# Performance work log

Hardware: AMD Instinct MI355X
Metric: run time of the kernel (lower is better)

The kernel has to match this reference:

```python
import jax, jax.numpy as jnp
import numpy as np

H = 64
N_PERSON = 200000
N_MOVIE = 100000
E_ACTED = 1600000
E_DIRECTED = 200000
E_WWW = 3200000
N_LAYERS = 2


def setup_inputs() -> dict:
    key = jax.random.key(0)
    ks = jax.random.split(key, 24)
    s = 1.0 / np.sqrt(H)
    inp = {
        "x_person": jax.random.normal(ks[0], (N_PERSON, H), jnp.float32),
        "x_movie": jax.random.normal(ks[1], (N_MOVIE, H), jnp.float32),
        "acted_src": jax.random.randint(ks[2], (E_ACTED,), 0, N_PERSON, jnp.int32),
        "acted_dst": jax.random.randint(ks[3], (E_ACTED,), 0, N_MOVIE, jnp.int32),
        "directed_src": jax.random.randint(ks[4], (E_DIRECTED,), 0, N_PERSON, jnp.int32),
        "directed_dst": jax.random.randint(ks[5], (E_DIRECTED,), 0, N_MOVIE, jnp.int32),
        "www_src": jax.random.randint(ks[6], (E_WWW,), 0, N_PERSON, jnp.int32),
        "www_dst": jax.random.randint(ks[7], (E_WWW,), 0, N_PERSON, jnp.int32),
        # per-relation SAGEConv params, stacked over the 2 layers
        "Wl_acted": jax.random.normal(ks[8], (N_LAYERS, H, H), jnp.float32) * s,
        "bl_acted": jnp.zeros((N_LAYERS, H), jnp.float32),
        "Wr_acted": jax.random.normal(ks[9], (N_LAYERS, H, H), jnp.float32) * s,
        "Wl_directed": jax.random.normal(ks[10], (N_LAYERS, H, H), jnp.float32) * s,
        "bl_directed": jnp.zeros((N_LAYERS, H), jnp.float32),
        "Wr_directed": jax.random.normal(ks[11], (N_LAYERS, H, H), jnp.float32) * s,
        "Wl_www": jax.random.normal(ks[12], (N_LAYERS, H, H), jnp.float32) * s,
        "bl_www": jnp.zeros((N_LAYERS, H), jnp.float32),
        "Wr_www": jax.random.normal(ks[13], (N_LAYERS, H, H), jnp.float32) * s,
        "lin_W": jax.random.normal(ks[14], (1, H), jnp.float32) * s,
        "lin_b": jnp.zeros((1,), jnp.float32),
    }
    return inp


def sage_conv(x_src, x_dst, src, dst, Wl, bl, Wr, n_dst):
    # PyG SAGEConv: mean-aggregate source feats at dst, then lin_l(agg) + lin_r(x_dst)
    agg = jax.ops.segment_sum(x_src[src], dst, num_segments=n_dst)  # [n_dst, H_in]
    cnt = jax.ops.segment_sum(jnp.ones((src.shape[0],), x_src.dtype), dst, num_segments=n_dst)
    mean = agg / jnp.maximum(cnt, 1.0)[:, None]
    return mean @ Wl.T + bl + x_dst @ Wr.T


def reference(x_person, x_movie, acted_src, acted_dst, directed_src, directed_dst,
              www_src, www_dst, Wl_acted, bl_acted, Wr_acted,
              Wl_directed, bl_directed, Wr_directed,
              Wl_www, bl_www, Wr_www, lin_W, lin_b):
    x_p, x_m = x_person, x_movie
    for l in range(N_LAYERS):
        # HeteroConv(aggr='sum'): movie receives sum of acted_in and directed convs
        out_m = sage_conv(x_p, x_m, acted_src, acted_dst,
                          Wl_acted[l], bl_acted[l], Wr_acted[l], N_MOVIE)
        out_m = out_m + sage_conv(x_p, x_m, directed_src, directed_dst,
                                  Wl_directed[l], bl_directed[l], Wr_directed[l], N_MOVIE)
        out_p = sage_conv(x_p, x_p, www_src, www_dst,
                          Wl_www[l], bl_www[l], Wr_www[l], N_PERSON)
        x_m = jax.nn.relu(out_m)
        x_p = jax.nn.relu(out_p)
    return (x_m @ lin_W.T + lin_b).squeeze(-1)  # [N_MOVIE]
```

## Files before the change

kernel.cpp:

```cpp
#include <hip/hip_runtime.h>

#define H 64
#define N_PERSON 200000
#define N_MOVIE 100000
#define E_ACTED 1600000
#define E_DIRECTED 200000
#define E_WWW 3200000
#define E_TOTAL (E_ACTED + E_DIRECTED + E_WWW)

#define SH 11
#define NBIN 2048
#define CH 16384

static __device__ __forceinline__ ushort f2bf(float f) {
  uint u = __float_as_uint(f);
  uint r = (u + 0x7FFFu + ((u >> 16) & 1u)) >> 16;
  return (ushort)r;
}
static __device__ __forceinline__ float bflo(uint u) { return __uint_as_float(u << 16); }
static __device__ __forceinline__ float bfhi(uint u) { return __uint_as_float(u & 0xFFFF0000u); }
static __device__ __forceinline__ float bfhiq(uint u) { return __uint_as_float(u); }
static __device__ __forceinline__ uint packbf(float lo, float hi) {
  return (uint)f2bf(lo) | ((uint)f2bf(hi) << 16);
}


struct RelP {
  const int* src; const int* dst; int* off;
  int E, N, nblk, nbuk, blkbase, bukbase, cbase, ebase;
};


static __global__ __launch_bounds__(256) void cast_all_k(const float* __restrict__ i0,
                                                         ushort* __restrict__ o0, int n0,
                                                         const float* __restrict__ i1,
                                                         ushort* __restrict__ o1, int n1) {
  int i = blockIdx.x * 256 + threadIdx.x;
  int stride = gridDim.x * 256;
  int nt = n0 + n1;
  for (; i < nt; i += stride) {
    const float4* in; ushort4* out; int idx;
    if (i < n0) { in = (const float4*)i0; out = (ushort4*)o0; idx = i; }
    else { in = (const float4*)i1; out = (ushort4*)o1; idx = i - n0; }
    float4 v = in[idx];
    ushort4 o;
    o.x = f2bf(v.x); o.y = f2bf(v.y); o.z = f2bf(v.z); o.w = f2bf(v.w);
    out[idx] = o;
  }
}


static __global__ __launch_bounds__(1024) void scan_block_k(const int* __restrict__ in, int n,
                                                            int* __restrict__ out,
                                                            int* __restrict__ partials) {
  __shared__ int sm[1024];
  int tid = threadIdx.x;
  int gid = blockIdx.x * 1024 + tid;
  int v = (gid < n) ? in[gid] : 0;
  sm[tid] = v;
  __syncthreads();
  for (int d = 1; d < 1024; d <<= 1) {
    int t = (tid >= d) ? sm[tid - d] : 0;
    __syncthreads();
    if (tid >= d) sm[tid] += t;
    __syncthreads();
  }
  if (gid < n) out[gid] = sm[tid] - v;
  if (tid == 1023 && partials) partials[blockIdx.x] = sm[1023];
}

static __global__ __launch_bounds__(1024) void add_off_k(int* __restrict__ off, int n,
                                                         const int* __restrict__ parts, int total) {
  int gid = blockIdx.x * 1024 + threadIdx.x;
  if (gid < n) off[gid] += parts[gid >> 10];
  else if (gid == n) off[gid] = total;
}


static __global__ __launch_bounds__(256) void part_count_all_k(RelP a, RelP b, RelP c,
                                                               int* __restrict__ counts) {
  __shared__ int hist[128];
  int blk = blockIdx.x, t = threadIdx.x;
  RelP r = (blk >= c.blkbase) ? c : (blk >= b.blkbase) ? b : a;
  int lb = blk - r.blkbase;
  for (int i = t; i < r.nbuk; i += 256) hist[i] = 0;
  __syncthreads();
  int e0 = lb * CH, e1 = min(e0 + CH, r.E);
  for (int e = e0 + t; e < e1; e += 256) atomicAdd(&hist[r.dst[e] >> SH], 1);
  __syncthreads();
  for (int i = t; i < r.nbuk; i += 256) counts[r.cbase + i * r.nblk + lb] = hist[i];
}

static __global__ __launch_bounds__(256) void part_scatter_all_k(RelP a, RelP b, RelP c,
                                                                 const int* __restrict__ off_bb,
                                                                 int* __restrict__ pairs) {
  __shared__ int cur[128];
  int blk = blockIdx.x, t = threadIdx.x;
  RelP r = (blk >= c.blkbase) ? c : (blk >= b.blkbase) ? b : a;
  int lb = blk - r.blkbase;
  for (int i = t; i < r.nbuk; i += 256) cur[i] = off_bb[r.cbase + i * r.nblk + lb];
  __syncthreads();
  int e0 = lb * CH, e1 = min(e0 + CH, r.E);
  int e = e0 + t;
  for (; e + 256 < e1; e += 512) {
    int d0 = r.dst[e], s0 = r.src[e];
    int d1 = r.dst[e + 256], s1 = r.src[e + 256];
    int p0 = atomicAdd(&cur[d0 >> SH], 1);
    int p1 = atomicAdd(&cur[d1 >> SH], 1);
    pairs[p0] = ((d0 & (NBIN - 1)) << 18) | s0;
    pairs[p1] = ((d1 & (NBIN - 1)) << 18) | s1;
  }
  if (e < e1) {
    int d0 = r.dst[e], s0 = r.src[e];
    int p0 = atomicAdd(&cur[d0 >> SH], 1);
    pairs[p0] = ((d0 & (NBIN - 1)) << 18) | s0;
  }
}

static __global__ __launch_bounds__(1024) void fine_sort_all_k(RelP a, RelP b, RelP c,
                                                               const int* __restrict__ off_bb,
                                                               const int* __restrict__ pairs,
                                                               int* __restrict__ csr) {
  __shared__ int hist[NBIN];
  __shared__ int sc[NBIN];
  int bb = blockIdx.x, t = threadIdx.x;
  RelP r = (bb >= c.bukbase) ? c : (bb >= b.bukbase) ? b : a;
  int bkt = bb - r.bukbase;
  int bstart = off_bb[r.cbase + bkt * r.nblk];
  int bend = (bkt + 1 < r.nbuk) ? off_bb[r.cbase + (bkt + 1) * r.nblk] : (r.ebase + r.E);
  int base = bkt << SH;
  hist[t] = 0; hist[t + 1024] = 0;
  __syncthreads();
  for (int e = bstart + t; e < bend; e += 1024) atomicAdd(&hist[((uint)pairs[e]) >> 18], 1);
  __syncthreads();
  sc[t] = hist[t]; sc[t + 1024] = hist[t + 1024];
  __syncthreads();
  for (int d = 1; d < NBIN; d <<= 1) {
    int v0 = (t >= d) ? sc[t - d] : 0;
    int v1 = (t + 1024 >= d) ? sc[t + 1024 - d] : 0;
    __syncthreads();
    sc[t] += v0; sc[t + 1024] += v1;
    __syncthreads();
  }
  int ex0 = sc[t] - hist[t];
  int ex1 = sc[t + 1024] - hist[t + 1024];
  if (base + t < r.N) r.off[base + t] = bstart + ex0;
  if (base + t + 1024 < r.N) r.off[base + t + 1024] = bstart + ex1;
  if (bkt == r.nbuk - 1 && t == 0) r.off[r.N] = r.ebase + r.E;
  hist[t] = ex0; hist[t + 1024] = ex1;
  __syncthreads();
  for (int e = bstart + t; e < bend; e += 1024) {
    int p = pairs[e];
    int pos = bstart + atomicAdd(&hist[((uint)p) >> 18], 1);
    csr[pos] = p & 0x3FFFF;
  }
}


struct PullT { const ushort* xsrc; const int* off; ushort* mean; int n; int blkbase; };

static __global__ __launch_bounds__(256) void pull_all_k(PullT t0, PullT t1, PullT t2,
                                                         const int* __restrict__ csr) {
  int blk = blockIdx.x;
  PullT tk;
  if (t2.n > 0 && blk >= t2.blkbase) tk = t2;
  else if (blk >= t1.blkbase) tk = t1;
  else tk = t0;
  int lane = threadIdx.x & 63;
  int g = lane >> 3;
  int fo = lane & 7;
  int d = ((blk - tk.blkbase) * 4 + (threadIdx.x >> 6)) * 8 + g;
  bool dok = d < tk.n;
  int dd = dok ? d : (tk.n - 1);
  int e0 = tk.off[dd];
  int e1 = tk.off[dd + 1];
  int cnt = dok ? (e1 - e0) : 0;
  int mx = cnt;
  mx = max(mx, __shfl_xor(mx, 8, 64));
  mx = max(mx, __shfl_xor(mx, 16, 64));
  mx = max(mx, __shfl_xor(mx, 32, 64));

  const ushort* __restrict__ xrow = tk.xsrc + fo * 8;
  float a0 = 0.f, a1 = 0.f, a2 = 0.f, a3 = 0.f, a4 = 0.f, a5 = 0.f, a6 = 0.f, a7 = 0.f;

  int i = 0;
  for (; i + 2 <= mx; i += 2) {
    if (i + 1 < cnt) {
      int s0 = csr[e0 + i];
      int s1 = csr[e0 + i + 1];
      uint4 u0 = *(const uint4*)(xrow + (size_t)s0 * 64);
      uint4 u1 = *(const uint4*)(xrow + (size_t)s1 * 64);
      a0 += bflo(u0.x); a1 += bfhiq(u0.x);
      a2 += bflo(u0.y); a3 += bfhiq(u0.y);
      a4 += bflo(u0.z); a5 += bfhiq(u0.z);
      a6 += bflo(u0.w); a7 += bfhiq(u0.w);
      a0 += bflo(u1.x); a1 += bfhiq(u1.x);
      a2 += bflo(u1.y); a3 += bfhiq(u1.y);
      a4 += bflo(u1.z); a5 += bfhiq(u1.z);
      a6 += bflo(u1.w); a7 += bfhiq(u1.w);
    } else if (i < cnt) {
      int s0 = csr[e0 + i];
      uint4 u0 = *(const uint4*)(xrow + (size_t)s0 * 64);
      a0 += bflo(u0.x); a1 += bfhiq(u0.x);
      a2 += bflo(u0.y); a3 += bfhiq(u0.y);
      a4 += bflo(u0.z); a5 += bfhiq(u0.z);
      a6 += bflo(u0.w); a7 += bfhiq(u0.w);
    }
  }
  if (i < mx && i < cnt) {
    int s0 = csr[e0 + i];
    uint4 u0 = *(const uint4*)(xrow + (size_t)s0 * 64);
    a0 += bflo(u0.x); a1 += bfhiq(u0.x);
    a2 += bflo(u0.y); a3 += bfhiq(u0.y);
    a4 += bflo(u0.z); a5 += bfhiq(u0.z);
    a6 += bflo(u0.w); a7 += bfhiq(u0.w);
  }

  if (dok) {
    float inv = 1.0f / fmaxf((float)cnt, 1.0f);
    uint4 o;
    o.x = packbf(a0 * inv, a1 * inv);
    o.y = packbf(a2 * inv, a3 * inv);
    o.z = packbf(a4 * inv, a5 * inv);
    o.w = packbf(a6 * inv, a7 * inv);
    *(uint4*)(tk.mean + (size_t)d * 64 + fo * 8) = o;
  }
}


struct GemmT {
  const ushort *A0, *A1, *A2;
  const float *W0, *W1, *W2, *Wadd, *b0, *b1;
  ushort* outB;
  const float *projW, *projb;
  float* projOut;
  int M, nsrc, blkbase;
};

static __global__ __launch_bounds__(256) void gemm_all_k(GemmT g0, GemmT g1) {
  GemmT g = (g1.M > 0 && (int)blockIdx.x >= g1.blkbase) ? g1 : g0;
  __shared__ float At[64 * 132];
  __shared__ float Wt[64 * 68];
  const ushort* As[3] = {g.A0, g.A1, g.A2};
  const float* Ws[3] = {g.W0, g.W1, g.W2};
  const int t = threadIdx.x;
  const int m0 = ((int)blockIdx.x - g.blkbase) * 128;
  const int tc = t & 15;
  const int tr = t >> 4;
  float acc[8][4];
#pragma unroll
  for (int r = 0; r < 8; ++r)
#pragma unroll
    for (int c = 0; c < 4; ++c) acc[r][c] = 0.f;

  for (int s = 0; s < g.nsrc; ++s) {
    if (s) __syncthreads();
    const float* W = Ws[s];
    const float* Wa = (s == g.nsrc - 1) ? g.Wadd : nullptr;
    for (int i = 0; i < 4; ++i) {
      int f = i * 256 + t;
      int j = f & 63;
      int c4 = f >> 6;
      float4 v = *(const float4*)(W + j * 64 + c4 * 4);
      if (Wa) {
        float4 v2 = *(const float4*)(Wa + j * 64 + c4 * 4);
        v.x += v2.x; v.y += v2.y; v.z += v2.z; v.w += v2.w;
      }
      Wt[(c4 * 4 + 0) * 68 + j] = v.x;
      Wt[(c4 * 4 + 1) * 68 + j] = v.y;
      Wt[(c4 * 4 + 2) * 68 + j] = v.z;
      Wt[(c4 * 4 + 3) * 68 + j] = v.w;
    }
    const ushort* A = As[s];
    for (int i = 0; i < 4; ++i) {
      int f = i * 256 + t;
      int row = f & 127;
      int c8 = f >> 7;
      int m = m0 + row;
      uint4 u = make_uint4(0, 0, 0, 0);
      if (m < g.M) u = *(const uint4*)(A + (size_t)m * 64 + c8 * 8);
      At[(c8 * 8 + 0) * 132 + row] = bflo(u.x);
      At[(c8 * 8 + 1) * 132 + row] = bfhi(u.x);
      At[(c8 * 8 + 2) * 132 + row] = bflo(u.y);
      At[(c8 * 8 + 3) * 132 + row] = bfhi(u.y);
      At[(c8 * 8 + 4) * 132 + row] = bflo(u.z);
      At[(c8 * 8 + 5) * 132 + row] = bfhi(u.z);
      At[(c8 * 8 + 6) * 132 + row] = bflo(u.w);
      At[(c8 * 8 + 7) * 132 + row] = bfhi(u.w);
    }
    __syncthreads();

#pragma unroll 8
    for (int k = 0; k < 64; ++k) {
      float4 w = *(const float4*)(&Wt[k * 68 + tc * 4]);
      float4 a0 = *(const float4*)(&At[k * 132 + tr * 8]);
      float4 a1 = *(const float4*)(&At[k * 132 + tr * 8 + 4]);
      float av[8] = {a0.x, a0.y, a0.z, a0.w, a1.x, a1.y, a1.z, a1.w};
      float wv[4] = {w.x, w.y, w.z, w.w};
#pragma unroll
      for (int r = 0; r < 8; ++r)
#pragma unroll
        for (int c = 0; c < 4; ++c) acc[r][c] = fmaf(av[r], wv[c], acc[r][c]);
    }
  }

  float4 bv = make_float4(0.f, 0.f, 0.f, 0.f);
  if (g.b0) {
    float4 b0 = *(const float4*)(g.b0 + tc * 4);
    bv.x += b0.x; bv.y += b0.y; bv.z += b0.z; bv.w += b0.w;
  }
  if (g.b1) {
    float4 b1 = *(const float4*)(g.b1 + tc * 4);
    bv.x += b1.x; bv.y += b1.y; bv.z += b1.z; bv.w += b1.w;
  }

  float4 pw = make_float4(0.f, 0.f, 0.f, 0.f);
  float pb = 0.f;
  if (g.projOut) {
    pw = *(const float4*)(g.projW + tc * 4);
    pb = g.projb[0];
  }

#pragma unroll
  for (int r = 0; r < 8; ++r) {
    int m = m0 + tr * 8 + r;
    if (m < g.M) {
      float4 o;
      o.x = fmaxf(acc[r][0] + bv.x, 0.f);
      o.y = fmaxf(acc[r][1] + bv.y, 0.f);
      o.z = fmaxf(acc[r][2] + bv.z, 0.f);
      o.w = fmaxf(acc[r][3] + bv.w, 0.f);
      if (g.projOut) {
        float p = o.x * pw.x + o.y * pw.y + o.z * pw.z + o.w * pw.w;
        p += __shfl_xor(p, 1, 64);
        p += __shfl_xor(p, 2, 64);
        p += __shfl_xor(p, 4, 64);
        p += __shfl_xor(p, 8, 64);
        if (tc == 0) g.projOut[m] = p + pb;
      } else {
        ushort4 ob;
        ob.x = f2bf(o.x); ob.y = f2bf(o.y); ob.z = f2bf(o.z); ob.w = f2bf(o.w);
        *(ushort4*)(g.outB + (size_t)m * 64 + tc * 4) = ob;
      }
    }
  }
}


extern "C" void kernel_launch(void* const* d_in, const int* in_sizes, int n_in, void* d_out,
                              int out_size, void* d_ws, size_t ws_size, hipStream_t stream) {
  const float* x_person = (const float*)d_in[0];
  const float* x_movie = (const float*)d_in[1];
  const int* acted_src = (const int*)d_in[2];
  const int* acted_dst = (const int*)d_in[3];
  const int* directed_src = (const int*)d_in[4];
  const int* directed_dst = (const int*)d_in[5];
  const int* www_src = (const int*)d_in[6];
  const int* www_dst = (const int*)d_in[7];
  const float* Wl_acted = (const float*)d_in[8];
  const float* bl_acted = (const float*)d_in[9];
  const float* Wr_acted = (const float*)d_in[10];
  const float* Wl_directed = (const float*)d_in[11];
  const float* bl_directed = (const float*)d_in[12];
  const float* Wr_directed = (const float*)d_in[13];
  const float* Wl_www = (const float*)d_in[14];
  const float* bl_www = (const float*)d_in[15];
  const float* Wr_www = (const float*)d_in[16];
  const float* lin_W = (const float*)d_in[17];
  const float* lin_b = (const float*)d_in[18];
  float* out = (float*)d_out;
  (void)in_sizes; (void)n_in; (void)out_size; (void)ws_size;

  char* base = (char*)d_ws;
  size_t pos = 0;
  auto carve = [&](size_t b) -> void* {
    void* r = base + pos;
    pos += (b + 255) & ~(size_t)255;
    return r;
  };
  int* off_a = (int*)carve((N_MOVIE + 1) * sizeof(int));
  int* off_d = (int*)carve((N_MOVIE + 1) * sizeof(int));
  int* off_w = (int*)carve((N_PERSON + 1) * sizeof(int));
  int* parts = (int*)carve(1024 * sizeof(int));
  int* csr_all = (int*)carve((size_t)E_TOTAL * sizeof(int));
  int* pairs = (int*)carve((size_t)E_TOTAL * sizeof(int));
  ushort* xpbf = (ushort*)carve((size_t)N_PERSON * H * sizeof(ushort));
  ushort* xmbf = (ushort*)carve((size_t)N_MOVIE * H * sizeof(ushort));
  ushort* xp0bf = (ushort*)carve((size_t)N_PERSON * H * sizeof(ushort));
  ushort* xm0bf = (ushort*)carve((size_t)N_MOVIE * H * sizeof(ushort));
  ushort* meanAbf = (ushort*)carve((size_t)N_MOVIE * H * sizeof(ushort));
  ushort* meanDbf = (ushort*)carve((size_t)N_MOVIE * H * sizeof(ushort));
  ushort* meanWbf = (ushort*)carve((size_t)N_PERSON * H * sizeof(ushort));

  RelP rA, rD, rW;
  rA.src = acted_src;  rA.dst = acted_dst;  rA.off = off_a;
  rA.E = E_ACTED;      rA.N = N_MOVIE;
  rA.nblk = (E_ACTED + CH - 1) / CH;      rA.nbuk = (N_MOVIE + NBIN - 1) >> SH;
  rD.src = directed_src; rD.dst = directed_dst; rD.off = off_d;
  rD.E = E_DIRECTED;     rD.N = N_MOVIE;
  rD.nblk = (E_DIRECTED + CH - 1) / CH;   rD.nbuk = (N_MOVIE + NBIN - 1) >> SH;
  rW.src = www_src;    rW.dst = www_dst;  rW.off = off_w;
  rW.E = E_WWW;        rW.N = N_PERSON;
  rW.nblk = (E_WWW + CH - 1) / CH;        rW.nbuk = (N_PERSON + NBIN - 1) >> SH;
  rA.blkbase = 0;                 rD.blkbase = rA.nblk;           rW.blkbase = rA.nblk + rD.nblk;
  rA.bukbase = 0;                 rD.bukbase = rA.nbuk;           rW.bukbase = rA.nbuk + rD.nbuk;
  rA.cbase = 0;                   rD.cbase = rA.nbuk * rA.nblk;
  rW.cbase = rD.cbase + rD.nbuk * rD.nblk;
  rA.ebase = 0;                   rD.ebase = E_ACTED;             rW.ebase = E_ACTED + E_DIRECTED;
  const int n_total = rW.cbase + rW.nbuk * rW.nblk;
  const int nblk_total = rW.blkbase + rW.nblk;
  const int nbuk_total = rW.bukbase + rW.nbuk;

  int* counts = (int*)carve((size_t)n_total * sizeof(int));
  int* off_bb = (int*)carve((size_t)(n_total + 1) * sizeof(int));

  part_count_all_k<<<nblk_total, 256, 0, stream>>>(rA, rD, rW, counts);
  int nb = (n_total + 1023) / 1024;
  scan_block_k<<<nb, 1024, 0, stream>>>(counts, n_total, off_bb, parts);
  scan_block_k<<<1, 1024, 0, stream>>>(parts, nb, parts, nullptr);
  add_off_k<<<(n_total + 1 + 1023) / 1024, 1024, 0, stream>>>(off_bb, n_total, parts, E_TOTAL);
  part_scatter_all_k<<<nblk_total, 256, 0, stream>>>(rA, rD, rW, off_bb, pairs);
  fine_sort_all_k<<<nbuk_total, 1024, 0, stream>>>(rA, rD, rW, off_bb, pairs, csr_all);

  cast_all_k<<<2048, 256, 0, stream>>>(x_person, xpbf, N_PERSON * H / 4, x_movie, xmbf,
                                       N_MOVIE * H / 4);

  const int nbA = (N_MOVIE + 31) / 32, nbD = (N_MOVIE + 31) / 32, nbW = (N_PERSON + 31) / 32;
  const int gmM = (N_MOVIE + 127) / 128, gmP = (N_PERSON + 127) / 128;

  {
    PullT pA = {xpbf, off_a, meanAbf, N_MOVIE, 0};
    PullT pD = {xpbf, off_d, meanDbf, N_MOVIE, nbA};
    PullT pW = {xpbf, off_w, meanWbf, N_PERSON, nbA + nbD};
    pull_all_k<<<nbA + nbD + nbW, 256, 0, stream>>>(pA, pD, pW, csr_all);
  }
  {
    GemmT gM = {meanAbf, meanDbf, xmbf,
                Wl_acted, Wl_directed, Wr_acted, Wr_directed, bl_acted, bl_directed,
                xm0bf, nullptr, nullptr, nullptr, N_MOVIE, 3, 0};
    GemmT gP = {meanWbf, xpbf, nullptr,
                Wl_www, Wr_www, nullptr, nullptr, bl_www, nullptr,
                xp0bf, nullptr, nullptr, nullptr, N_PERSON, 2, gmM};
    gemm_all_k<<<gmM + gmP, 256, 0, stream>>>(gM, gP);
  }
  {
    PullT pA = {xp0bf, off_a, meanAbf, N_MOVIE, 0};
    PullT pD = {xp0bf, off_d, meanDbf, N_MOVIE, nbA};
    PullT pZ = {nullptr, nullptr, nullptr, 0, 0};
    pull_all_k<<<nbA + nbD, 256, 0, stream>>>(pA, pD, pZ, csr_all);
  }
  {
    GemmT gM = {meanAbf, meanDbf, xm0bf,
                Wl_acted + 4096, Wl_directed + 4096, Wr_acted + 4096, Wr_directed + 4096,
                bl_acted + 64, bl_directed + 64,
                nullptr, lin_W, lin_b, out, N_MOVIE, 3, 0};
    GemmT gZ = {nullptr, nullptr, nullptr, nullptr, nullptr, nullptr, nullptr, nullptr, nullptr,
                nullptr, nullptr, nullptr, nullptr, 0, 0, 0};
    gemm_all_k<<<gmM, 256, 0, stream>>>(gM, gZ);
  }
}
```

Baseline: 421.1 us.

## Rewrite fused SAGE GEMM with bf16 MFMA and 256-row tiles

Replaces the scalar FP32 FMA GEMM, which converted A to fp32 in LDS, with MFMA 16x16x32 bf16 instructions. A fragments are loaded straight from global memory and only the weights are staged in LDS, as bf16, for all sources at once. Each block now covers 256 rows instead of 128, so fewer blocks are launched and weights are restaged less often. Weights are now rounded to bf16, which lowers precision, and the pull-kernel macro is only a cleanup.

```diff
diff --git a/kernel.cpp b/kernel.cpp
--- a/kernel.cpp
+++ b/kernel.cpp
@@ -12,13 +12,15 @@
 #define NBIN 2048
 #define CH 16384
 
+typedef __attribute__((ext_vector_type(8))) short bf16x8;
+typedef __attribute__((ext_vector_type(4))) float f32x4;
+
 static __device__ __forceinline__ ushort f2bf(float f) {
   uint u = __float_as_uint(f);
   uint r = (u + 0x7FFFu + ((u >> 16) & 1u)) >> 16;
   return (ushort)r;
 }
 static __device__ __forceinline__ float bflo(uint u) { return __uint_as_float(u << 16); }
-static __device__ __forceinline__ float bfhi(uint u) { return __uint_as_float(u & 0xFFFF0000u); }
 static __device__ __forceinline__ float bfhiq(uint u) { return __uint_as_float(u); }
 static __device__ __forceinline__ uint packbf(float lo, float hi) {
   return (uint)f2bf(lo) | ((uint)f2bf(hi) << 16);
@@ -158,6 +160,14 @@
 
 
 struct PullT { const ushort* xsrc; const int* off; ushort* mean; int n; int blkbase; };
+
+#define ACC8(u)                                  \
+  do {                                           \
+    a0 += bflo((u).x); a1 += bfhiq((u).x);       \
+    a2 += bflo((u).y); a3 += bfhiq((u).y);       \
+    a4 += bflo((u).z); a5 += bfhiq((u).z);       \
+    a6 += bflo((u).w); a7 += bfhiq((u).w);       \
+  } while (0)
 
 static __global__ __launch_bounds__(256) void pull_all_k(PullT t0, PullT t1, PullT t2,
                                                          const int* __restrict__ csr) {
@@ -190,30 +200,17 @@
       int s1 = csr[e0 + i + 1];
       uint4 u0 = *(const uint4*)(xrow + (size_t)s0 * 64);
       uint4 u1 = *(const uint4*)(xrow + (size_t)s1 * 64);
-      a0 += bflo(u0.x); a1 += bfhiq(u0.x);
-      a2 += bflo(u0.y); a3 += bfhiq(u0.y);
-      a4 += bflo(u0.z); a5 += bfhiq(u0.z);
-      a6 += bflo(u0.w); a7 += bfhiq(u0.w);
-      a0 += bflo(u1.x); a1 += bfhiq(u1.x);
-      a2 += bflo(u1.y); a3 += bfhiq(u1.y);
-      a4 += bflo(u1.z); a5 += bfhiq(u1.z);
-      a6 += bflo(u1.w); a7 += bfhiq(u1.w);
+      ACC8(u0); ACC8(u1);
     } else if (i < cnt) {
       int s0 = csr[e0 + i];
       uint4 u0 = *(const uint4*)(xrow + (size_t)s0 * 64);
-      a0 += bflo(u0.x); a1 += bfhiq(u0.x);
-      a2 += bflo(u0.y); a3 += bfhiq(u0.y);
-      a4 += bflo(u0.z); a5 += bfhiq(u0.z);
-      a6 += bflo(u0.w); a7 += bfhiq(u0.w);
+      ACC8(u0);
     }
   }
   if (i < mx && i < cnt) {
     int s0 = csr[e0 + i];
     uint4 u0 = *(const uint4*)(xrow + (size_t)s0 * 64);
-    a0 += bflo(u0.x); a1 += bfhiq(u0.x);
-    a2 += bflo(u0.y); a3 += bfhiq(u0.y);
-    a4 += bflo(u0.z); a5 += bfhiq(u0.z);
-    a6 += bflo(u0.w); a7 += bfhiq(u0.w);
+    ACC8(u0);
   }
 
   if (dok) {
@@ -239,108 +236,106 @@
 
 static __global__ __launch_bounds__(256) void gemm_all_k(GemmT g0, GemmT g1) {
   GemmT g = (g1.M > 0 && (int)blockIdx.x >= g1.blkbase) ? g1 : g0;
-  __shared__ float At[64 * 132];
-  __shared__ float Wt[64 * 68];
-  const ushort* As[3] = {g.A0, g.A1, g.A2};
-  const float* Ws[3] = {g.W0, g.W1, g.W2};
+  __shared__ ushort Wt[3][64][72];
   const int t = threadIdx.x;
-  const int m0 = ((int)blockIdx.x - g.blkbase) * 128;
-  const int tc = t & 15;
-  const int tr = t >> 4;
-  float acc[8][4];
-#pragma unroll
-  for (int r = 0; r < 8; ++r)
-#pragma unroll
-    for (int c = 0; c < 4; ++c) acc[r][c] = 0.f;
-
-  for (int s = 0; s < g.nsrc; ++s) {
-    if (s) __syncthreads();
-    const float* W = Ws[s];
-    const float* Wa = (s == g.nsrc - 1) ? g.Wadd : nullptr;
-    for (int i = 0; i < 4; ++i) {
-      int f = i * 256 + t;
-      int j = f & 63;
-      int c4 = f >> 6;
-      float4 v = *(const float4*)(W + j * 64 + c4 * 4);
+  const int w = t >> 6;
+  const int l = t & 63;
+  const int lr = l & 15;
+  const int lk = l >> 4;
+  const int m0 = ((int)blockIdx.x - g.blkbase) * 256;
+
+  auto stageW = [&](const float* W, int s, const float* Wa) {
+#pragma unroll
+    for (int i = 0; i < 8; ++i) {
+      int dp = t + i * 256;
+      int j = dp >> 5;
+      int kk = (dp & 31) * 2;
+      float2 wv = *(const float2*)(W + j * 64 + kk);
       if (Wa) {
-        float4 v2 = *(const float4*)(Wa + j * 64 + c4 * 4);
-        v.x += v2.x; v.y += v2.y; v.z += v2.z; v.w += v2.w;
+        float2 av = *(const float2*)(Wa + j * 64 + kk);
+        wv.x += av.x; wv.y += av.y;
       }
-      Wt[(c4 * 4 + 0) * 68 + j] = v.x;
-      Wt[(c4 * 4 + 1) * 68 + j] = v.y;
-      Wt[(c4 * 4 + 2) * 68 + j] = v.z;
-      Wt[(c4 * 4 + 3) * 68 + j] = v.w;
-    }
-    const ushort* A = As[s];
-    for (int i = 0; i < 4; ++i) {
-      int f = i * 256 + t;
-      int row = f & 127;
-      int c8 = f >> 7;
-      int m = m0 + row;
-      uint4 u = make_uint4(0, 0, 0, 0);
-      if (m < g.M) u = *(const uint4*)(A + (size_t)m * 64 + c8 * 8);
-      At[(c8 * 8 + 0) * 132 + row] = bflo(u.x);
-      At[(c8 * 8 + 1) * 132 + row] = bfhi(u.x);
-      At[(c8 * 8 + 2) * 132 + row] = bflo(u.y);
-      At[(c8 * 8 + 3) * 132 + row] = bfhi(u.y);
-      At[(c8 * 8 + 4) * 132 + row] = bflo(u.z);
-      At[(c8 * 8 + 5) * 132 + row] = bfhi(u.z);
-      At[(c8 * 8 + 6) * 132 + row] = bflo(u.w);
-      At[(c8 * 8 + 7) * 132 + row] = bfhi(u.w);
-    }
-    __syncthreads();
-
-#pragma unroll 8
-    for (int k = 0; k < 64; ++k) {
-      float4 w = *(const float4*)(&Wt[k * 68 + tc * 4]);
-      float4 a0 = *(const float4*)(&At[k * 132 + tr * 8]);
-      float4 a1 = *(const float4*)(&At[k * 132 + tr * 8 + 4]);
-      float av[8] = {a0.x, a0.y, a0.z, a0.w, a1.x, a1.y, a1.z, a1.w};
-      float wv[4] = {w.x, w.y, w.z, w.w};
-#pragma unroll
-      for (int r = 0; r < 8; ++r)
-#pragma unroll
-        for (int c = 0; c < 4; ++c) acc[r][c] = fmaf(av[r], wv[c], acc[r][c]);
-    }
-  }
-
-  float4 bv = make_float4(0.f, 0.f, 0.f, 0.f);
-  if (g.b0) {
-    float4 b0 = *(const float4*)(g.b0 + tc * 4);
-    bv.x += b0.x; bv.y += b0.y; bv.z += b0.z; bv.w += b0.w;
-  }
-  if (g.b1) {
-    float4 b1 = *(const float4*)(g.b1 + tc * 4);
-    bv.x += b1.x; bv.y += b1.y; bv.z += b1.z; bv.w += b1.w;
-  }
-
-  float4 pw = make_float4(0.f, 0.f, 0.f, 0.f);
-  float pb = 0.f;
+      *(uint*)&Wt[s][j][kk] = packbf(wv.x, wv.y);
+    }
+  };
+  stageW(g.W0, 0, nullptr);
+  stageW(g.W1, 1, g.nsrc == 2 ? g.Wadd : nullptr);
+  if (g.nsrc > 2) stageW(g.W2, 2, g.Wadd);
+  __syncthreads();
+
+  f32x4 acc[4][4];
+#pragma unroll
+  for (int mt = 0; mt < 4; ++mt)
+#pragma unroll
+    for (int jt = 0; jt < 4; ++jt) acc[mt][jt] = (f32x4){0.f, 0.f, 0.f, 0.f};
+
+  auto doSrc = [&](const ushort* A, int s) {
+    bf16x8 aF[4][2];
+#pragma unroll
+    for (int mt = 0; mt < 4; ++mt) {
+      int m = m0 + w * 64 + mt * 16 + lr;
+      const ushort* ap = A + (size_t)(m < g.M ? m : 0) * 64 + lk * 8;
+      aF[mt][0] = *(const bf16x8*)(ap);
+      aF[mt][1] = *(const bf16x8*)(ap + 32);
+    }
+#pragma unroll
+    for (int jt = 0; jt < 4; ++jt) {
+#pragma unroll
+      for (int k0 = 0; k0 < 2; ++k0) {
+        bf16x8 bF = *(const bf16x8*)&Wt[s][jt * 16 + lr][k0 * 32 + lk * 8];
+#pragma unroll
+        for (int mt = 0; mt < 4; ++mt)
+          acc[mt][jt] =
+              __builtin_amdgcn_mfma_f32_16x16x32_bf16(bF, aF[mt][k0], acc[mt][jt], 0, 0, 0);
+      }
+    }
+  };
+  doSrc(g.A0, 0);
+  doSrc(g.A1, 1);
+  if (g.nsrc > 2) doSrc(g.A2, 2);
+
+  f32x4 bv[4];
+#pragma unroll
+  for (int jt = 0; jt < 4; ++jt) {
+    f32x4 b = (f32x4){0.f, 0.f, 0.f, 0.f};
+    if (g.b0) b += *(const f32x4*)(g.b0 + jt * 16 + lk * 4);
+    if (g.b1) b += *(const f32x4*)(g.b1 + jt * 16 + lk * 4);
+    bv[jt] = b;
+  }
+
   if (g.projOut) {
-    pw = *(const float4*)(g.projW + tc * 4);
-    pb = g.projb[0];
-  }
-
-#pragma unroll
-  for (int r = 0; r < 8; ++r) {
-    int m = m0 + tr * 8 + r;
-    if (m < g.M) {
-      float4 o;
-      o.x = fmaxf(acc[r][0] + bv.x, 0.f);
-      o.y = fmaxf(acc[r][1] + bv.y, 0.f);
-      o.z = fmaxf(acc[r][2] + bv.z, 0.f);
-      o.w = fmaxf(acc[r][3] + bv.w, 0.f);
-      if (g.projOut) {
-        float p = o.x * pw.x + o.y * pw.y + o.z * pw.z + o.w * pw.w;
-        p += __shfl_xor(p, 1, 64);
-        p += __shfl_xor(p, 2, 64);
-        p += __shfl_xor(p, 4, 64);
-        p += __shfl_xor(p, 8, 64);
-        if (tc == 0) g.projOut[m] = p + pb;
-      } else {
-        ushort4 ob;
-        ob.x = f2bf(o.x); ob.y = f2bf(o.y); ob.z = f2bf(o.z); ob.w = f2bf(o.w);
-        *(ushort4*)(g.outB + (size_t)m * 64 + tc * 4) = ob;
+    f32x4 pw[4];
+#pragma unroll
+    for (int jt = 0; jt < 4; ++jt) pw[jt] = *(const f32x4*)(g.projW + jt * 16 + lk * 4);
+    float pb = g.projb[0];
+#pragma unroll
+    for (int mt = 0; mt < 4; ++mt) {
+      float p = 0.f;
+#pragma unroll
+      for (int jt = 0; jt < 4; ++jt) {
+        f32x4 o = acc[mt][jt] + bv[jt];
+#pragma unroll
+        for (int q = 0; q < 4; ++q) p += fmaxf(o[q], 0.f) * pw[jt][q];
+      }
+      p += __shfl_xor(p, 16, 64);
+      p += __shfl_xor(p, 32, 64);
+      int m = m0 + w * 64 + mt * 16 + lr;
+      if (lk == 0 && m < g.M) g.projOut[m] = p + pb;
+    }
+  } else {
+#pragma unroll
+    for (int mt = 0; mt < 4; ++mt) {
+      int m = m0 + w * 64 + mt * 16 + lr;
+      if (m < g.M) {
+        ushort* row = g.outB + (size_t)m * 64 + lk * 4;
+#pragma unroll
+        for (int jt = 0; jt < 4; ++jt) {
+          f32x4 o = acc[mt][jt] + bv[jt];
+          uint2 pk;
+          pk.x = packbf(fmaxf(o[0], 0.f), fmaxf(o[1], 0.f));
+          pk.y = packbf(fmaxf(o[2], 0.f), fmaxf(o[3], 0.f));
+          *(uint2*)(row + jt * 16) = pk;
+        }
       }
     }
   }
@@ -426,7 +421,7 @@
                                        N_MOVIE * H / 4);
 
   const int nbA = (N_MOVIE + 31) / 32, nbD = (N_MOVIE + 31) / 32, nbW = (N_PERSON + 31) / 32;
-  const int gmM = (N_MOVIE + 127) / 128, gmP = (N_PERSON + 127) / 128;
+  const int gmM = (N_MOVIE + 255) / 256, gmP = (N_PERSON + 255) / 256;
 
   {
     PullT pA = {xpbf, off_a, meanAbf, N_MOVIE, 0};
```

Result: faster. 344.3 us (-18.2%).
